# Performance work log

Measured on AMD Instinct MI355X. Metric: run time of the kernel, lower is better.

## Reference

```python
import jax, jax.numpy as jnp
import numpy as np

N_HEAD = 16

def setup_inputs() -> dict:
    key = jax.random.key(0)
    k0, k1, k2, k3, k4 = jax.random.split(key, 5)
    B, T, C = 4, 2048, 1024
    x = jax.random.normal(k0, (B, T, C), dtype=jnp.float32)
    # torch nn.Linear weights are (out_features, in_features); scale like kaiming-uniform-ish
    s = 1.0 / np.sqrt(C)
    Wk = jax.random.uniform(k1, (C, C), jnp.float32, -s, s)
    Wq = jax.random.uniform(k2, (C, C), jnp.float32, -s, s)
    Wv = jax.random.uniform(k3, (C, C), jnp.float32, -s, s)
    Wo = jax.random.uniform(k4, (C, C), jnp.float32, -s, s)
    return {"x": x, "Wk": Wk, "Wq": Wq, "Wv": Wv, "Wo": Wo}

def reference(x, Wk, Wq, Wv, Wo):
    B, T, C = x.shape
    hs = C // N_HEAD
    # projections (torch Linear: y = x @ W.T), split heads -> (B, nh, T, hs)
    def proj(W):
        return (x @ W.T).reshape(B, T, N_HEAD, hs).transpose(0, 2, 1, 3)
    k = proj(Wk)
    q = proj(Wq)
    v = proj(Wv)
    # dot attention: scale by sqrt(head_dim) (k.shape[2] after transpose in source)
    score = jnp.einsum('bhqd,bhkd->bhqk', q, k) / jnp.sqrt(jnp.asarray(hs, x.dtype))
    # NOTE: source calls score.masked_fill(mask, -inf) without assignment -> mask has no effect.
    e = jax.nn.softmax(score, axis=-1)
    o = jnp.einsum('bhqk,bhkd->bhqd', e, v)          # (B, nh, T, hs)
    o = o.transpose(0, 2, 1, 3).reshape(B, T, C)     # merge heads
    o = o @ Wo.T                                      # final projection
    # dropout is identity in eval mode
    return o
```

## Files before the change

### kernel.cpp

```cpp
#include <hip/hip_runtime.h>
#include <hip/hip_bf16.h>
#include <cstddef>
#include <cstdint>

#define B_DIM 4
#define T_DIM 2048
#define C_DIM 1024
#define NHEAD 16
#define HS    64
#define QKV_LD 3072

#define QSCALE 0.18033688011112042f

typedef __attribute__((ext_vector_type(8))) short short8;
typedef __attribute__((ext_vector_type(4))) float f32x4;

__device__ __forceinline__ short f2bf(float x) {
    __hip_bfloat16 b = __float2bfloat16(x);
    return *reinterpret_cast<short*>(&b);
}

__device__ __forceinline__ void load_lds16(const void* g, void* l) {
    __builtin_amdgcn_global_load_lds(
        (const __attribute__((address_space(1))) void*)(g),
        (__attribute__((address_space(3))) void*)(l),
        16, 0, 0);
}

__global__ __launch_bounds__(256) void cast_bf16(
    const float* __restrict__ in, short* __restrict__ out, int n8, float scale)
{
    int i = blockIdx.x * 256 + threadIdx.x;
    if (i >= n8) return;
    const float4* p = (const float4*)in + (size_t)i * 2;
    float4 a = p[0], b = p[1];
    short8 o;
    o[0]=f2bf(a.x*scale); o[1]=f2bf(a.y*scale); o[2]=f2bf(a.z*scale); o[3]=f2bf(a.w*scale);
    o[4]=f2bf(b.x*scale); o[5]=f2bf(b.y*scale); o[6]=f2bf(b.z*scale); o[7]=f2bf(b.w*scale);
    *((short8*)out + i) = o;
}

__global__ __launch_bounds__(256) void cast4_bf16(
    const float* __restrict__ w0, const float* __restrict__ w1,
    const float* __restrict__ w2, const float* __restrict__ w3,
    short* __restrict__ out, int n8)
{
    int i = blockIdx.x * 256 + threadIdx.x;
    if (i >= n8) return;
    const int sel = blockIdx.y;
    const float* in = (sel == 0) ? w0 : (sel == 1) ? w1 : (sel == 2) ? w2 : w3;
    const float scale = (sel == 0) ? QSCALE : 1.0f;
    const float4* p = (const float4*)in + (size_t)i * 2;
    float4 a = p[0], b = p[1];
    short8 o;
    o[0]=f2bf(a.x*scale); o[1]=f2bf(a.y*scale); o[2]=f2bf(a.z*scale); o[3]=f2bf(a.w*scale);
    o[4]=f2bf(b.x*scale); o[5]=f2bf(b.y*scale); o[6]=f2bf(b.z*scale); o[7]=f2bf(b.w*scale);
    *((short8*)out + (size_t)sel * n8 + i) = o;
}

template<bool OUT_BF16>
__global__ __launch_bounds__(512, 2) void gemm_bt_8ph(
    const short* __restrict__ A,
    const short* __restrict__ Bm,
    void* __restrict__ Cm,
    int M, int N, int K)
{
    __shared__ __align__(16) short lds[49152];

    const int nbx = N >> 8;
    int wg = blockIdx.x;
    const int cpx = gridDim.x >> 3;
    wg = (wg & 7) * cpx + (wg >> 3);
    const int bx = wg % nbx, by = wg / nbx;
    const int m0 = by << 7, n0 = bx << 8;

    const int t = threadIdx.x;
    const int w = t >> 6, lane = t & 63;
    const int l16 = lane & 15, quad = lane >> 4;
    const int wm = w >> 2, wn = w & 3;

    const int rcall  = t >> 3;
    const int schunk = (t & 7) ^ (rcall & 7);
    const int dstoff = w * 512;

    const short* Ag = A  + (size_t)(m0 + rcall) * K + schunk * 8;
    const short* Bg = Bm + (size_t)(n0 + rcall) * K + schunk * 8;

    short* const Ab0 = lds;
    short* const Ab1 = lds + 8192;
    short* const Bb0 = lds + 16384;
    short* const Bb1 = lds + 32768;

    int aoff[4][2], boff[4][2];
    #pragma unroll
    for (int mf = 0; mf < 4; ++mf) {
        const int ar = wm * 64 + mf * 16 + l16;
        #pragma unroll
        for (int ks = 0; ks < 2; ++ks)
            aoff[mf][ks] = ar * 64 + (((ks * 4 + quad) ^ (ar & 7)) * 8);
    }
    #pragma unroll
    for (int nf = 0; nf < 4; ++nf) {
        const int br = wn * 64 + nf * 16 + l16;
        #pragma unroll
        for (int ks = 0; ks < 2; ++ks)
            boff[nf][ks] = br * 64 + (((ks * 4 + quad) ^ (br & 7)) * 8);
    }

    f32x4 acc[4][4];
    const f32x4 zero4 = {0.f, 0.f, 0.f, 0.f};
    #pragma unroll
    for (int mf = 0; mf < 4; ++mf)
        #pragma unroll
        for (int nf = 0; nf < 4; ++nf) acc[mf][nf] = zero4;

    const int NT = K >> 6;

    #define ST64(gb, kt, ro, lb)                                               \
        load_lds16((gb) + (size_t)(ro) * K + (size_t)(kt) * 64,                \
                   (lb) + (ro) * 64 + dstoff)

    ST64(Ag, 0, 0, Ab0); ST64(Ag, 0, 64, Ab0);
    ST64(Bg, 0, 0, Bb0); ST64(Bg, 0, 64, Bb0);
    ST64(Bg, 0, 128, Bb0); ST64(Bg, 0, 192, Bb0);
    ST64(Ag, 1, 0, Ab1); ST64(Ag, 1, 64, Ab1);

    for (int kt = 0; kt < NT; ++kt) {
        short* Acur = (kt & 1) ? Ab1 : Ab0;
        short* Bcur = (kt & 1) ? Bb1 : Bb0;
        short* Bnx  = (kt & 1) ? Bb0 : Bb1;

        if (kt == NT - 1) asm volatile("s_waitcnt vmcnt(0)" ::: "memory");
        else              asm volatile("s_waitcnt vmcnt(2)" ::: "memory");
        __builtin_amdgcn_s_barrier();

        short8 bfr[4][2], af[2][2];
        #pragma unroll
        for (int nf = 0; nf < 4; ++nf)
            #pragma unroll
            for (int ks = 0; ks < 2; ++ks)
                bfr[nf][ks] = *(const short8*)(Bcur + boff[nf][ks]);
        #pragma unroll
        for (int mf = 0; mf < 2; ++mf)
            #pragma unroll
            for (int ks = 0; ks < 2; ++ks)
                af[mf][ks] = *(const short8*)(Acur + aoff[mf][ks]);

        if (kt + 1 < NT) { ST64(Bg, kt + 1, 0, Bnx); ST64(Bg, kt + 1, 64, Bnx); }

        __builtin_amdgcn_s_barrier();
        __builtin_amdgcn_s_setprio(1);
        #pragma unroll
        for (int mf = 0; mf < 2; ++mf)
            #pragma unroll
            for (int nf = 0; nf < 4; ++nf)
                #pragma unroll
                for (int ks = 0; ks < 2; ++ks)
                    acc[mf][nf] = __builtin_amdgcn_mfma_f32_16x16x32_bf16(
                        af[mf][ks], bfr[nf][ks], acc[mf][nf], 0, 0, 0);
        __builtin_amdgcn_s_setprio(0);
        __builtin_amdgcn_s_barrier();

        short8 af2[2][2];
        #pragma unroll
        for (int mf = 0; mf < 2; ++mf)
            #pragma unroll
            for (int ks = 0; ks < 2; ++ks)
                af2[mf][ks] = *(const short8*)(Acur + aoff[2 + mf][ks]);

        if (kt + 1 < NT) { ST64(Bg, kt + 1, 128, Bnx); ST64(Bg, kt + 1, 192, Bnx); }

        __builtin_amdgcn_s_barrier();
        __builtin_amdgcn_s_setprio(1);
        #pragma unroll
        for (int mf = 0; mf < 2; ++mf)
            #pragma unroll
            for (int nf = 0; nf < 4; ++nf)
                #pragma unroll
                for (int ks = 0; ks < 2; ++ks)
                    acc[2 + mf][nf] = __builtin_amdgcn_mfma_f32_16x16x32_bf16(
                        af2[mf][ks], bfr[nf][ks], acc[2 + mf][nf], 0, 0, 0);
        __builtin_amdgcn_s_setprio(0);
        __builtin_amdgcn_s_barrier();

        if (kt + 2 < NT) {
            short* Aw = (kt & 1) ? Ab1 : Ab0;
            ST64(Ag, kt + 2, 0, Aw); ST64(Ag, kt + 2, 64, Aw);
        }
    }
    #undef ST64

    #pragma unroll
    for (int mf = 0; mf < 4; ++mf) {
        const int row_base = m0 + wm * 64 + mf * 16 + quad * 4;
        #pragma unroll
        for (int nf = 0; nf < 4; ++nf) {
            const int col = n0 + wn * 64 + nf * 16 + l16;
            #pragma unroll
            for (int r = 0; r < 4; ++r) {
                const size_t idx = (size_t)(row_base + r) * N + col;
                if (OUT_BF16) ((short*)Cm)[idx] = f2bf(acc[mf][nf][r]);
                else          ((float*)Cm)[idx] = acc[mf][nf][r];
            }
        }
    }
}

__global__ __launch_bounds__(256) void transpose_v(
    const short* __restrict__ Vb,
    short* __restrict__ Vt, int srcLD)
{
    const int t0 = blockIdx.x * 64;
    const int head = blockIdx.y;
    const int b = head >> 4, h = head & 15;

    __shared__ short Ls[64][72];

    const int t = threadIdx.x;
    const int r = t >> 2;
    const int c = (t & 3) * 16;

    const short* src = Vb + ((size_t)(b * T_DIM) + t0 + r) * srcLD + h * HS + c;
    *(short8*)&Ls[r][c]     = *(const short8*)src;
    *(short8*)&Ls[r][c + 8] = *(const short8*)(src + 8);
    __syncthreads();

    short tmp[16];
    #pragma unroll
    for (int i = 0; i < 16; ++i) tmp[i] = Ls[c + i][r];
    short* dst = Vt + ((size_t)head * HS + r) * T_DIM + t0 + c;
    *(short8*)dst       = *(short8*)&tmp[0];
    *(short8*)(dst + 8) = *(short8*)&tmp[8];
}

#define QSUB 4

__global__ __launch_bounds__(256, 2) void attn_mfma3(
    const short* __restrict__ Qb,
    const short* __restrict__ Kb,
    const short* __restrict__ Vt,
    short* __restrict__ O)
{
    const int i0   = blockIdx.x * (64 * QSUB);
    const int head = blockIdx.y;
    const int b = head >> 4, h = head & 15;

    const int t    = threadIdx.x;
    const int w    = t >> 6;
    const int lane = t & 63;
    const int l16  = lane & 15;
    const int quad = lane >> 4;

    __shared__ __align__(16) short Ks[64][64];
    __shared__ __align__(16) short Vts[64][64];

    short8 qf[QSUB][2];
    #pragma unroll
    for (int sub = 0; sub < QSUB; ++sub) {
        const short* qrow = Qb
            + ((size_t)(b * T_DIM) + i0 + sub * 64 + w * 16 + l16) * QKV_LD + h * HS;
        qf[sub][0] = *(const short8*)(qrow + quad * 8);
        qf[sub][1] = *(const short8*)(qrow + 32 + quad * 8);
    }

    short8 onesv;
    #pragma unroll
    for (int j = 0; j < 8; ++j) onesv[j] = (short)0x3F80;

    const f32x4 zero4 = {0.f, 0.f, 0.f, 0.f};
    f32x4 oacc[QSUB][4];
    f32x4 lacc[QSUB];
    #pragma unroll
    for (int sub = 0; sub < QSUB; ++sub) {
        #pragma unroll
        for (int dg = 0; dg < 4; ++dg) oacc[sub][dg] = zero4;
        lacc[sub] = zero4;
    }

    const int sr  = t >> 2;
    const int sc2 = (t & 3) * 2;
    const int krow = (sr & 32) | ((sr & 4) << 2) | ((sr & 24) >> 1) | (sr & 3);
    const short* kgbase = Kb + (size_t)(b * T_DIM) * QKV_LD + h * HS;
    const short* vgbase = Vt + ((size_t)head * HS + sr) * T_DIM;

    short* kd0 = &Ks[krow][((sc2    ) ^ (krow & 7)) * 8];
    short* kd1 = &Ks[krow][((sc2 + 1) ^ (krow & 7)) * 8];
    short* vd0 = &Vts[sr][((sc2    ) ^ (sr & 7)) * 8];
    short* vd1 = &Vts[sr][((sc2 + 1) ^ (sr & 7)) * 8];

    const int x7 = l16 & 7;

    for (int j0 = 0; j0 < T_DIM; j0 += 64) {
        __syncthreads();
        {
            const short* kp = kgbase + (size_t)(j0 + sr) * QKV_LD + sc2 * 8;
            *(short8*)kd0 = *(const short8*)kp;
            *(short8*)kd1 = *(const short8*)(kp + 8);
            const short* vp = vgbase + j0 + sc2 * 8;
            *(short8*)vd0 = *(const short8*)vp;
            *(short8*)vd1 = *(const short8*)(vp + 8);
        }
        __syncthreads();

        short8 ka[4][2], va[4][2];
        #pragma unroll
        for (int kt = 0; kt < 4; ++kt) {
            const int row = kt * 16 + l16;
            ka[kt][0] = *(const short8*)&Ks[row][((quad    ) ^ x7) * 8];
            ka[kt][1] = *(const short8*)&Ks[row][((quad + 4) ^ x7) * 8];
            va[kt][0] = *(const short8*)&Vts[row][((quad    ) ^ x7) * 8];
            va[kt][1] = *(const short8*)&Vts[row][((quad + 4) ^ x7) * 8];
        }

        #pragma unroll
        for (int sub = 0; sub < QSUB; ++sub) {
            f32x4 s[4];
            #pragma unroll
            for (int kt = 0; kt < 4; ++kt) {
                f32x4 acc = zero4;
                acc = __builtin_amdgcn_mfma_f32_16x16x32_bf16(ka[kt][0], qf[sub][0], acc, 0, 0, 0);
                acc = __builtin_amdgcn_mfma_f32_16x16x32_bf16(ka[kt][1], qf[sub][1], acc, 0, 0, 0);
                s[kt] = acc;
            }

            short8 pa[2];
            #pragma unroll
            for (int hh = 0; hh < 2; ++hh) {
                #pragma unroll
                for (int c = 0; c < 2; ++c) {
                    f32x4 sv = s[2 * hh + c];
                    #pragma unroll
                    for (int r = 0; r < 4; ++r) {
                        float p = __builtin_amdgcn_exp2f(sv[r]);
                        pa[hh][c * 4 + r] = f2bf(p);
                    }
                }
            }

            lacc[sub] = __builtin_amdgcn_mfma_f32_16x16x32_bf16(pa[0], onesv, lacc[sub], 0, 0, 0);
            lacc[sub] = __builtin_amdgcn_mfma_f32_16x16x32_bf16(pa[1], onesv, lacc[sub], 0, 0, 0);

            #pragma unroll
            for (int dg = 0; dg < 4; ++dg) {
                oacc[sub][dg] = __builtin_amdgcn_mfma_f32_16x16x32_bf16(pa[0], va[dg][0], oacc[sub][dg], 0, 0, 0);
                oacc[sub][dg] = __builtin_amdgcn_mfma_f32_16x16x32_bf16(pa[1], va[dg][1], oacc[sub][dg], 0, 0, 0);
            }
        }
    }

    #pragma unroll
    for (int sub = 0; sub < QSUB; ++sub) {
        float linv[4];
        #pragma unroll
        for (int r = 0; r < 4; ++r) linv[r] = 1.0f / lacc[sub][r];

        #pragma unroll
        for (int r = 0; r < 4; ++r) {
            short* orow = O + ((size_t)(b * T_DIM) + i0 + sub * 64 + w * 16 + quad * 4 + r) * C_DIM + h * HS;
            #pragma unroll
            for (int dg = 0; dg < 4; ++dg)
                orow[dg * 16 + l16] = f2bf(oacc[sub][dg][r] * linv[r]);
        }
    }
}

extern "C" void kernel_launch(void* const* d_in, const int* in_sizes, int n_in,
                              void* d_out, int out_size, void* d_ws, size_t ws_size,
                              hipStream_t stream) {
    const float* x  = (const float*)d_in[0];
    const float* Wk = (const float*)d_in[1];
    const float* Wq = (const float*)d_in[2];
    const float* Wv = (const float*)d_in[3];
    const float* Wo = (const float*)d_in[4];
    float* out = (float*)d_out;

    const int M = B_DIM * T_DIM;
    const size_t NE = (size_t)M * C_DIM;
    const size_t NB = 2 * NE;
    const size_t WB = (size_t)2 * C_DIM * C_DIM;
    const size_t WE = (size_t)C_DIM * C_DIM;

    char* ws = (char*)d_ws;
    short* xb   = (short*)(ws);
    short* Ob   = xb;
    short* QKVb = (short*)(ws + NB);
    short* Vtb  = (short*)(ws + 4 * NB);
    short* W3b  = (short*)(ws + 5 * NB);
    short* Wob  = (short*)(ws + 5 * NB + 3 * WB);

    cast_bf16<<<(int)(NE / 8 / 256), 256, 0, stream>>>(x, xb, (int)(NE / 8), 1.0f);
    const int wn8 = (int)(WE / 8);
    cast4_bf16<<<dim3(wn8 / 256, 4), 256, 0, stream>>>(Wq, Wk, Wv, Wo, W3b, wn8);

    gemm_bt_8ph<true><<<dim3((QKV_LD / 256) * (M / 128)), 512, 0, stream>>>(
        xb, W3b, QKVb, M, QKV_LD, C_DIM);

    transpose_v<<<dim3(T_DIM / 64, B_DIM * NHEAD), 256, 0, stream>>>(
        QKVb + 2 * C_DIM, Vtb, QKV_LD);

    attn_mfma3<<<dim3(T_DIM / (64 * QSUB), B_DIM * NHEAD), 256, 0, stream>>>(
        QKVb, QKVb + C_DIM, Vtb, Ob);

    gemm_bt_8ph<false><<<dim3((C_DIM / 256) * (M / 128)), 512, 0, stream>>>(
        Ob, Wob, out, M, C_DIM, C_DIM);
}
```

Measured before the change: 253.5 us.

## Halve query subtiles, raise occupancy, and replace XOR swizzle with padded LDS

```diff
diff --git a/kernel.cpp b/kernel.cpp
--- a/kernel.cpp
+++ b/kernel.cpp
@@ -233,9 +233,9 @@
     *(short8*)(dst + 8) = *(short8*)&tmp[8];
 }
 
-#define QSUB 4
-
-__global__ __launch_bounds__(256, 2) void attn_mfma3(
+#define QSUB 2
+
+__global__ __launch_bounds__(256, 4) void attn_mfma3(
     const short* __restrict__ Qb,
     const short* __restrict__ Kb,
     const short* __restrict__ Vt,
@@ -251,8 +251,8 @@
     const int l16  = lane & 15;
     const int quad = lane >> 4;
 
-    __shared__ __align__(16) short Ks[64][64];
-    __shared__ __align__(16) short Vts[64][64];
+    __shared__ short Ks[64][72];
+    __shared__ short Vts[64][72];
 
     short8 qf[QSUB][2];
     #pragma unroll
@@ -277,39 +277,31 @@
         lacc[sub] = zero4;
     }
 
-    const int sr  = t >> 2;
-    const int sc2 = (t & 3) * 2;
+    const int sr = t >> 2;
+    const int sc = (t & 3) * 16;
     const int krow = (sr & 32) | ((sr & 4) << 2) | ((sr & 24) >> 1) | (sr & 3);
     const short* kgbase = Kb + (size_t)(b * T_DIM) * QKV_LD + h * HS;
     const short* vgbase = Vt + ((size_t)head * HS + sr) * T_DIM;
 
-    short* kd0 = &Ks[krow][((sc2    ) ^ (krow & 7)) * 8];
-    short* kd1 = &Ks[krow][((sc2 + 1) ^ (krow & 7)) * 8];
-    short* vd0 = &Vts[sr][((sc2    ) ^ (sr & 7)) * 8];
-    short* vd1 = &Vts[sr][((sc2 + 1) ^ (sr & 7)) * 8];
-
-    const int x7 = l16 & 7;
-
     for (int j0 = 0; j0 < T_DIM; j0 += 64) {
         __syncthreads();
         {
-            const short* kp = kgbase + (size_t)(j0 + sr) * QKV_LD + sc2 * 8;
-            *(short8*)kd0 = *(const short8*)kp;
-            *(short8*)kd1 = *(const short8*)(kp + 8);
-            const short* vp = vgbase + j0 + sc2 * 8;
-            *(short8*)vd0 = *(const short8*)vp;
-            *(short8*)vd1 = *(const short8*)(vp + 8);
+            const short* kp = kgbase + (size_t)(j0 + sr) * QKV_LD + sc;
+            *(short8*)&Ks[krow][sc]     = *(const short8*)kp;
+            *(short8*)&Ks[krow][sc + 8] = *(const short8*)(kp + 8);
+            const short* vp = vgbase + j0 + sc;
+            *(short8*)&Vts[sr][sc]      = *(const short8*)vp;
+            *(short8*)&Vts[sr][sc + 8]  = *(const short8*)(vp + 8);
         }
         __syncthreads();
 
         short8 ka[4][2], va[4][2];
         #pragma unroll
         for (int kt = 0; kt < 4; ++kt) {
-            const int row = kt * 16 + l16;
-            ka[kt][0] = *(const short8*)&Ks[row][((quad    ) ^ x7) * 8];
-            ka[kt][1] = *(const short8*)&Ks[row][((quad + 4) ^ x7) * 8];
-            va[kt][0] = *(const short8*)&Vts[row][((quad    ) ^ x7) * 8];
-            va[kt][1] = *(const short8*)&Vts[row][((quad + 4) ^ x7) * 8];
+            ka[kt][0] = *(const short8*)&Ks[kt * 16 + l16][quad * 8];
+            ka[kt][1] = *(const short8*)&Ks[kt * 16 + l16][32 + quad * 8];
+            va[kt][0] = *(const short8*)&Vts[kt * 16 + l16][quad * 8];
+            va[kt][1] = *(const short8*)&Vts[kt * 16 + l16][32 + quad * 8];
         }
 
         #pragma unroll
```

Measured after the change: 259.6 us. +2.4%, slower.
